# Performance work log

Hardware: AMD Instinct MI355X
Metric: run time of the kernel (lower is better)

The kernel has to match this reference:

```python
import jax, jax.numpy as jnp
import numpy as np

B, L, D, H = 8, 256, 512, 512
NEG_BIG = 1e8  # matches the 100000000.0 mask constant in the original


def setup_inputs() -> dict:
    key = jax.random.key(0)
    k1, k2, k3, k4 = jax.random.split(key, 4)
    enc = jax.random.normal(k1, (B, L, D), dtype=jnp.float32)
    # Glorot-uniform init, matching tf.keras.initializers.GlorotUniform
    s_w = float(np.sqrt(6.0 / (D + H)))
    W_l = jax.random.uniform(k2, (D, H), jnp.float32, -s_w, s_w)
    W_r = jax.random.uniform(k3, (D, H), jnp.float32, -s_w, s_w)
    s_u = float(np.sqrt(6.0 / (H + H)))  # 1-D glorot: fan_in = fan_out = H
    U = jax.random.uniform(k4, (H,), jnp.float32, -s_u, s_u)
    logit_bias = jnp.zeros((1,), jnp.float32)  # bias_initial_value=None -> zeros init
    return {"encoder_output": enc, "W_l": W_l, "W_r": W_r, "U": U, "logit_bias": logit_bias}


def reference(encoder_output, W_l, W_r, U, logit_bias):
    # dot_l[b,i,h], dot_r[b,j,h]
    dot_l = jnp.einsum('bik,kh->bih', encoder_output, W_l)
    dot_r = jnp.einsum('bjk,kh->bjh', encoder_output, W_r)
    # additive biaffine: tanh(dot_l_i + dot_r_j) . U  -> logits[b,i,j]
    final_sum = jnp.tanh(dot_l[:, :, None, :] + dot_r[:, None, :, :])  # [B,L,L,H]
    logits = jnp.einsum('bijh,h->bij', final_sum, U) + logit_bias[0]   # [B,L,L]
    # per-row self-mask (one_hot(i)) applied over all rows at once
    masked = logits - NEG_BIG * jnp.eye(L, dtype=logits.dtype)[None]   # [B,L,L]
    # original returns python lists over i of [B,L]; stack -> [L,B,L]
    mask_scores = jnp.transpose(masked, (1, 0, 2))
    p = jax.nn.sigmoid(mask_scores)
    samples = jax.random.bernoulli(jax.random.key(42), p).astype(jnp.int32)  # [L,B,L]
    # Bernoulli entropy from logits x: p*softplus(-x) + (1-p)*softplus(x)
    entropy = p * jax.nn.softplus(-mask_scores) + (1.0 - p) * jax.nn.softplus(mask_scores)
    return samples, mask_scores, entropy
```

## Files before the change

kernel.cpp:

```cpp
#include <hip/hip_runtime.h>
#include <stdint.h>

#define Bb 8
#define Ll 256
#define Dd 512
#define Hh 512
#define Nout (Ll * Bb * Ll)

#define Kc 2.8853900817779268

#define RNG_PARTITIONABLE 1

typedef __attribute__((ext_vector_type(8))) short bf16x8;
typedef __attribute__((ext_vector_type(4))) float f32x4;

__device__ __forceinline__ uint32_t rotl32(uint32_t v, int s) {
  return (v << s) | (v >> (32 - s));
}
__device__ __forceinline__ void tf_round(uint32_t& x0, uint32_t& x1, int r) {
  x0 += x1;
  x1 = rotl32(x1, r);
  x1 ^= x0;
}
__device__ __forceinline__ uint2 threefry2x32_k042(uint32_t x0, uint32_t x1) {
  const uint32_t k0 = 0u;
  const uint32_t k1 = 42u;
  const uint32_t k2 = 0x1BD11BDAu ^ k0 ^ k1;
  x0 += k0; x1 += k1;
  tf_round(x0, x1, 13); tf_round(x0, x1, 15); tf_round(x0, x1, 26); tf_round(x0, x1, 6);
  x0 += k1; x1 += k2 + 1u;
  tf_round(x0, x1, 17); tf_round(x0, x1, 29); tf_round(x0, x1, 16); tf_round(x0, x1, 24);
  x0 += k2; x1 += k0 + 2u;
  tf_round(x0, x1, 13); tf_round(x0, x1, 15); tf_round(x0, x1, 26); tf_round(x0, x1, 6);
  x0 += k0; x1 += k1 + 3u;
  tf_round(x0, x1, 17); tf_round(x0, x1, 29); tf_round(x0, x1, 16); tf_round(x0, x1, 24);
  x0 += k1; x1 += k2 + 4u;
  tf_round(x0, x1, 13); tf_round(x0, x1, 15); tf_round(x0, x1, 26); tf_round(x0, x1, 6);
  x0 += k2; x1 += k0 + 5u;
  return make_uint2(x0, x1);
}

__device__ __forceinline__ uint32_t rng_bits(uint32_t n) {
#if RNG_PARTITIONABLE
  uint2 o = threefry2x32_k042(0u, n);
  return o.x ^ o.y;
#else
  const uint32_t half = (uint32_t)(Nout / 2);
  if (n < half) {
    uint2 o = threefry2x32_k042(n, n + half);
    return o.x;
  } else {
    uint2 o = threefry2x32_k042(n - half, n);
    return o.y;
  }
#endif
}

__device__ __forceinline__ unsigned short bf16_rne(float f) {
  uint32_t u = __float_as_uint(f);
  u = (u + 0x7fffu + ((u >> 16) & 1u)) >> 16;
  return (unsigned short)u;
}
__device__ __forceinline__ float bf16_tof(unsigned short h) {
  return __uint_as_float(((uint32_t)h) << 16);
}
__device__ __forceinline__ void split3(float a, unsigned short& h,
                                       unsigned short& m, unsigned short& l) {
  h = bf16_rne(a);
  const float r1 = a - bf16_tof(h);
  m = bf16_rne(r1);
  const float r2 = r1 - bf16_tof(m);
  l = bf16_rne(r2);
}

__global__ __launch_bounds__(256) void split_enc(
    const float* __restrict__ enc, unsigned short* __restrict__ ah,
    unsigned short* __restrict__ am, unsigned short* __restrict__ al) {
  const int idx = (blockIdx.x * 256 + threadIdx.x) * 4;
  const float4 v = *(const float4*)(enc + idx);
  ushort4 h4, m4, l4;
  split3(v.x, h4.x, m4.x, l4.x);
  split3(v.y, h4.y, m4.y, l4.y);
  split3(v.z, h4.z, m4.z, l4.z);
  split3(v.w, h4.w, m4.w, l4.w);
  *(ushort4*)(ah + idx) = h4;
  *(ushort4*)(am + idx) = m4;
  *(ushort4*)(al + idx) = l4;
}

__global__ __launch_bounds__(256) void split_wt(
    const float* __restrict__ Wl, const float* __restrict__ Wr,
    unsigned short* __restrict__ wh, unsigned short* __restrict__ wm,
    unsigned short* __restrict__ wl) {
  const int z = blockIdx.z;
  const float* W = z ? Wr : Wl;
  const size_t zo = (size_t)z * Hh * Dd;
  const int k0 = blockIdx.x * 64;
  const int n0 = blockIdx.y * 64;
  __shared__ float tile[64][65];

  const int t = threadIdx.x;
#pragma unroll
  for (int rep = 0; rep < 4; ++rep) {
    const int idx = t + rep * 256;
    const int r = idx >> 4;
    const int c = (idx & 15) * 4;
    const float4 v = *(const float4*)(W + (size_t)(k0 + r) * Hh + n0 + c);
    tile[r][c + 0] = v.x; tile[r][c + 1] = v.y;
    tile[r][c + 2] = v.z; tile[r][c + 3] = v.w;
  }
  __syncthreads();
#pragma unroll
  for (int rep = 0; rep < 4; ++rep) {
    const int idx = t + rep * 256;
    const int rr = idx >> 4;
    const int cc = (idx & 15) * 4;
    ushort4 h4, m4, l4;
    split3(tile[cc + 0][rr], h4.x, m4.x, l4.x);
    split3(tile[cc + 1][rr], h4.y, m4.y, l4.y);
    split3(tile[cc + 2][rr], h4.z, m4.z, l4.z);
    split3(tile[cc + 3][rr], h4.w, m4.w, l4.w);
    const size_t o = zo + (size_t)(n0 + rr) * Dd + k0 + cc;
    *(ushort4*)(wh + o) = h4;
    *(ushort4*)(wm + o) = m4;
    *(ushort4*)(wl + o) = l4;
  }
}

__global__ __launch_bounds__(256) void gemm_mfma(
    const unsigned short* __restrict__ ah, const unsigned short* __restrict__ am,
    const unsigned short* __restrict__ al, const unsigned short* __restrict__ wh,
    const unsigned short* __restrict__ wm, const unsigned short* __restrict__ wl,
    float* __restrict__ el, float* __restrict__ er) {
  const int flat = blockIdx.x;
  const int xcd = flat & 7;
  const int loc = flat >> 3;
  const int z = loc >> 5;
  const int ni = (loc >> 2) & 7;
  const int mi = (xcd << 2) | (loc & 3);
  const size_t zo = (size_t)z * Hh * Dd;
  float* C = z ? er : el;
  const int m0 = mi * 64;
  const int n0 = ni * 64;

  __shared__ unsigned short Asm[3][12 * 512];
  __shared__ unsigned short Bsm[3][12 * 512];

  const int t = threadIdx.x;
  const int lane = t & 63;
  const int wv = t >> 6;
  const int l15 = lane & 15;
  const int kq8 = (lane >> 4) * 8;

  const unsigned short* gp[6];
  size_t go[6];
  int lq[6];
  bool isA[6];
#pragma unroll
  for (int s = 0; s < 6; ++s) {
    const int q = wv * 6 + s;
    if (q < 12) {
      const int p = q >> 2, mt = q & 3;
      gp[s] = (p == 0) ? ah : (p == 1) ? am : al;
      go[s] = (size_t)(m0 + mt * 16 + l15) * Dd + kq8;
      lq[s] = q * 512;
      isA[s] = true;
    } else {
      const int q2 = q - 12;
      const int p = q2 >> 2, nt = q2 & 3;
      gp[s] = (p == 0) ? wh : (p == 1) ? wm : wl;
      go[s] = zo + (size_t)(n0 + nt * 16 + l15) * Dd + kq8;
      lq[s] = q2 * 512;
      isA[s] = false;
    }
  }

  auto stage = [&](int buf, int kc) {
    const int k0 = kc * 32;
#pragma unroll
    for (int s = 0; s < 6; ++s) {
      unsigned short* dst = isA[s] ? &Asm[buf][lq[s]] : &Bsm[buf][lq[s]];
      __builtin_amdgcn_global_load_lds(
          (const __attribute__((address_space(1))) void*)(gp[s] + go[s] + k0),
          (__attribute__((address_space(3))) void*)dst, 16, 0, 0);
    }
  };

  const int mp = wv & 1;
  const int np = wv >> 1;

  f32x4 acc[2][2][2];
#pragma unroll
  for (int mi2 = 0; mi2 < 2; ++mi2)
#pragma unroll
    for (int ni2 = 0; ni2 < 2; ++ni2)
#pragma unroll
      for (int hf = 0; hf < 2; ++hf) acc[mi2][ni2][hf] = (f32x4){0.f, 0.f, 0.f, 0.f};

  stage(0, 0);
  stage(1, 1);

#pragma unroll
  for (int kc = 0; kc < 16; ++kc) {
    const int buf = kc % 3;
    if (kc + 2 < 16) stage((kc + 2) % 3, kc + 2);

    if (kc <= 13) {
      asm volatile("s_waitcnt vmcnt(12)" ::: "memory");
    } else if (kc == 14) {
      asm volatile("s_waitcnt vmcnt(6)" ::: "memory");
    } else {
      asm volatile("s_waitcnt vmcnt(0)" ::: "memory");
    }
    __builtin_amdgcn_s_barrier();
    __builtin_amdgcn_sched_barrier(0);

    bf16x8 af[2][3], bfr[2][3];
#pragma unroll
    for (int mi2 = 0; mi2 < 2; ++mi2)
#pragma unroll
      for (int p = 0; p < 3; ++p)
        af[mi2][p] = *(const bf16x8*)&Asm[buf][(p * 4 + mp * 2 + mi2) * 512 + lane * 8];
#pragma unroll
    for (int ni2 = 0; ni2 < 2; ++ni2)
#pragma unroll
      for (int p = 0; p < 3; ++p)
        bfr[ni2][p] = *(const bf16x8*)&Bsm[buf][(p * 4 + np * 2 + ni2) * 512 + lane * 8];

    const int hf = kc >> 3;
#pragma unroll
    for (int mi2 = 0; mi2 < 2; ++mi2)
#pragma unroll
      for (int ni2 = 0; ni2 < 2; ++ni2) {
        f32x4 A = acc[mi2][ni2][hf];
        A = __builtin_amdgcn_mfma_f32_16x16x32_bf16(af[mi2][0], bfr[ni2][0], A, 0, 0, 0);
        A = __builtin_amdgcn_mfma_f32_16x16x32_bf16(af[mi2][0], bfr[ni2][1], A, 0, 0, 0);
        A = __builtin_amdgcn_mfma_f32_16x16x32_bf16(af[mi2][1], bfr[ni2][0], A, 0, 0, 0);
        A = __builtin_amdgcn_mfma_f32_16x16x32_bf16(af[mi2][0], bfr[ni2][2], A, 0, 0, 0);
        A = __builtin_amdgcn_mfma_f32_16x16x32_bf16(af[mi2][2], bfr[ni2][0], A, 0, 0, 0);
        A = __builtin_amdgcn_mfma_f32_16x16x32_bf16(af[mi2][1], bfr[ni2][1], A, 0, 0, 0);
        acc[mi2][ni2][hf] = A;
      }

    asm volatile("s_waitcnt lgkmcnt(0)" ::: "memory");
    __builtin_amdgcn_sched_barrier(0);
    __builtin_amdgcn_s_barrier();
  }

  const int rbase = (lane >> 4) * 4;
#pragma unroll
  for (int mi2 = 0; mi2 < 2; ++mi2) {
    const int mbase = m0 + (mp * 2 + mi2) * 16 + rbase;
#pragma unroll
    for (int ni2 = 0; ni2 < 2; ++ni2) {
      const int n = n0 + (np * 2 + ni2) * 16 + l15;
#pragma unroll
      for (int reg = 0; reg < 4; ++reg) {
        const double s = (double)acc[mi2][ni2][0][reg] + (double)acc[mi2][ni2][1][reg];
        C[(size_t)(mbase + reg) * Hh + n] = __builtin_amdgcn_exp2f((float)(Kc * s));
      }
    }
  }
}

__device__ __forceinline__ void group4_acc(float& S, const float4 a,
                                           const float4 bv, const float4 u) {
  const float d0 = __builtin_fmaf(a.x, bv.x, 1.0f);
  const float d1 = __builtin_fmaf(a.y, bv.y, 1.0f);
  const float d2 = __builtin_fmaf(a.z, bv.z, 1.0f);
  const float d3 = __builtin_fmaf(a.w, bv.w, 1.0f);
  const float p01 = d0 * d1;
  const float p23 = d2 * d3;
  const float D = p01 * p23;
  float n01 = u.x * d1;
  n01 = __builtin_fmaf(u.y, d0, n01);
  float n23 = u.z * d3;
  n23 = __builtin_fmaf(u.w, d2, n23);
  float num = n01 * p23;
  num = __builtin_fmaf(n23, p01, num);
  S = __builtin_fmaf(num, __builtin_amdgcn_rcpf(D), S);
}

__global__ __launch_bounds__(256) void biaffine_part(
    const float* __restrict__ el, const float* __restrict__ er,
    const float* __restrict__ U, float* __restrict__ part) {
  const int flat = blockIdx.x;
  const int b = flat & 7;
  const int loc = flat >> 3;
  const int ks = loc >> 4;
  const int ib = (loc >> 2) & 3;
  const int jb = loc & 3;
  const int i0 = ib * 64;
  const int j0 = jb * 64;
  const int h0 = ks * 64;

  __shared__ float els[64][68];
  __shared__ float ers[64][68];
  __shared__ float us[64];

  const int t = threadIdx.x;
  if (t < 16) *(float4*)&us[t * 4] = *(const float4*)(U + h0 + t * 4);

  const float* elg = el + (size_t)(b * Ll + i0) * Hh + h0;
  const float* erg = er + (size_t)(b * Ll + j0) * Hh + h0;
#pragma unroll
  for (int rep = 0; rep < 4; ++rep) {
    const int idx = t + rep * 256;
    const int r = idx >> 4;
    const int c = (idx & 15) * 4;
    *(float4*)&els[r][c] = *(const float4*)(elg + (size_t)r * Hh + c);
    *(float4*)&ers[r][c] = *(const float4*)(erg + (size_t)r * Hh + c);
  }
  __syncthreads();

  float usl = 0.0f;
#pragma unroll
  for (int q = 0; q < 16; ++q) {
    const float4 u = *(const float4*)&us[q * 4];
    usl += ((u.x + u.y) + u.z) + u.w;
  }

  const int ti = t >> 4;
  const int tj = t & 15;

  float S[4][4];
#pragma unroll
  for (int r = 0; r < 4; ++r)
#pragma unroll
    for (int c = 0; c < 4; ++c) S[r][c] = 0.0f;

  for (int g = 0; g < 16; ++g) {
    const int h = g * 4;
    const float4 u = *(const float4*)&us[h];
    float4 av[4], bv[4];
#pragma unroll
    for (int c = 0; c < 4; ++c) {
      av[c] = *(const float4*)&els[ti + 16 * c][h];
      bv[c] = *(const float4*)&ers[tj + 16 * c][h];
    }
#pragma unroll
    for (int r = 0; r < 4; ++r)
#pragma unroll
      for (int c = 0; c < 4; ++c) group4_acc(S[r][c], av[r], bv[c], u);
  }

  float* pslice = part + (size_t)ks * Nout;
#pragma unroll
  for (int r = 0; r < 4; ++r) {
    const int i = i0 + ti + 16 * r;
#pragma unroll
    for (int c = 0; c < 4; ++c) {
      const int j = j0 + tj + 16 * c;
      const uint32_t n = ((uint32_t)i * Bb + (uint32_t)b) * Ll + (uint32_t)j;
      pslice[n] = __builtin_fmaf(-2.0f, S[r][c], usl);
    }
  }
}

__global__ __launch_bounds__(256) void biaffine_emit(
    const float* __restrict__ part, const float* __restrict__ biasp,
    float* __restrict__ out) {
  const uint32_t n4 = (blockIdx.x * 256u + threadIdx.x) * 4u;
  double s0 = 0.0, s1 = 0.0, s2 = 0.0, s3 = 0.0;
#pragma unroll
  for (int k = 0; k < 8; ++k) {
    const float4 v = *(const float4*)(part + (size_t)k * Nout + n4);
    s0 += (double)v.x;
    s1 += (double)v.y;
    s2 += (double)v.z;
    s3 += (double)v.w;
  }
  const float bias = biasp[0];
  const double sv[4] = {s0, s1, s2, s3};

  float4 samp4, x4, ent4;
  float* sp = &samp4.x;
  float* xp = &x4.x;
  float* ep = &ent4.x;
#pragma unroll
  for (int q = 0; q < 4; ++q) {
    const uint32_t n = n4 + q;
    const int i = (int)(n >> 11);
    const int j = (int)(n & 255u);
    float x = (float)sv[q] + bias;
    if (i == j) x -= 1e8f;

    const double pd = 1.0 / (1.0 + exp(-(double)x));
    const float pf = (float)pd;

    const uint32_t bits = rng_bits(n);
    const float uu = __uint_as_float((bits >> 9) | 0x3f800000u) - 1.0f;
    sp[q] = (uu < pf) ? 1.0f : 0.0f;
    xp[q] = x;

    const float ax = fabsf(x);
    const float l1p = log1pf(expf(-ax));
    const float sp_pos = fmaxf(x, 0.0f) + l1p;
    const float sp_neg = fmaxf(-x, 0.0f) + l1p;
    ep[q] = pf * sp_neg + (1.0f - pf) * sp_pos;
  }
  *(float4*)(out + n4) = samp4;
  *(float4*)(out + Nout + n4) = x4;
  *(float4*)(out + 2 * (size_t)Nout + n4) = ent4;
}

extern "C" void kernel_launch(void* const* d_in, const int* in_sizes, int n_in,
                              void* d_out, int out_size, void* d_ws,
                              size_t ws_size, hipStream_t stream) {
  const float* enc = (const float*)d_in[0];
  const float* Wl = (const float*)d_in[1];
  const float* Wr = (const float*)d_in[2];
  const float* U = (const float*)d_in[3];
  const float* lb = (const float*)d_in[4];
  float* out = (float*)d_out;

  char* w = (char*)d_ws;
  float* el = (float*)w;                      w += (size_t)Bb * Ll * Hh * 4;
  float* er = (float*)w;                      w += (size_t)Bb * Ll * Hh * 4;
  float* part = (float*)w;                    w += (size_t)8 * Nout * 4;
  unsigned short* ah = (unsigned short*)w;    w += (size_t)Bb * Ll * Dd * 2;
  unsigned short* am = (unsigned short*)w;    w += (size_t)Bb * Ll * Dd * 2;
  unsigned short* al = (unsigned short*)w;    w += (size_t)Bb * Ll * Dd * 2;
  unsigned short* wh = (unsigned short*)w;    w += (size_t)2 * Dd * Hh * 2;
  unsigned short* wm = (unsigned short*)w;    w += (size_t)2 * Dd * Hh * 2;
  unsigned short* wl = (unsigned short*)w;    w += (size_t)2 * Dd * Hh * 2;

  split_enc<<<dim3((Bb * Ll * Dd) / 1024), 256, 0, stream>>>(enc, ah, am, al);
  split_wt<<<dim3(Dd / 64, Hh / 64, 2), 256, 0, stream>>>(Wl, Wr, wh, wm, wl);
  gemm_mfma<<<dim3(512, 1, 1), 256, 0, stream>>>(
      ah, am, al, wh, wm, wl, el, er);
  biaffine_part<<<dim3(1024, 1, 1), 256, 0, stream>>>(el, er, U, part);
  biaffine_emit<<<dim3(Nout / 1024), 256, 0, stream>>>(part, lb, out);
}
```

Before: 125.6 us.

## Split GEMM K dimension across two blocks and combine partials in biaffine kernel

```diff
diff --git a/kernel.cpp b/kernel.cpp
--- a/kernel.cpp
+++ b/kernel.cpp
@@ -6,6 +6,7 @@
 #define Dd 512
 #define Hh 512
 #define Nout (Ll * Bb * Ll)
+#define HALFSZ ((size_t)Bb * Ll * Hh)
 
 #define Kc 2.8853900817779268
 
@@ -131,20 +132,22 @@
     const unsigned short* __restrict__ ah, const unsigned short* __restrict__ am,
     const unsigned short* __restrict__ al, const unsigned short* __restrict__ wh,
     const unsigned short* __restrict__ wm, const unsigned short* __restrict__ wl,
-    float* __restrict__ el, float* __restrict__ er) {
+    float* __restrict__ elp, float* __restrict__ erp) {
   const int flat = blockIdx.x;
   const int xcd = flat & 7;
-  const int loc = flat >> 3;
+  const int half = (flat >> 3) & 1;
+  const int loc = flat >> 4;
   const int z = loc >> 5;
   const int ni = (loc >> 2) & 7;
   const int mi = (xcd << 2) | (loc & 3);
   const size_t zo = (size_t)z * Hh * Dd;
-  float* C = z ? er : el;
+  float* C = (z ? erp : elp) + (size_t)half * HALFSZ;
   const int m0 = mi * 64;
   const int n0 = ni * 64;
-
-  __shared__ unsigned short Asm[3][12 * 512];
-  __shared__ unsigned short Bsm[3][12 * 512];
+  const int kh0 = half * 256;
+
+  __shared__ unsigned short Asm[2][12 * 512];
+  __shared__ unsigned short Bsm[2][12 * 512];
 
   const int t = threadIdx.x;
   const int lane = t & 63;
@@ -176,7 +179,7 @@
   }
 
   auto stage = [&](int buf, int kc) {
-    const int k0 = kc * 32;
+    const int k0 = kh0 + kc * 32;
 #pragma unroll
     for (int s = 0; s < 6; ++s) {
       unsigned short* dst = isA[s] ? &Asm[buf][lq[s]] : &Bsm[buf][lq[s]];
@@ -189,25 +192,20 @@
   const int mp = wv & 1;
   const int np = wv >> 1;
 
-  f32x4 acc[2][2][2];
+  f32x4 acc[2][2];
 #pragma unroll
   for (int mi2 = 0; mi2 < 2; ++mi2)
 #pragma unroll
-    for (int ni2 = 0; ni2 < 2; ++ni2)
-#pragma unroll
-      for (int hf = 0; hf < 2; ++hf) acc[mi2][ni2][hf] = (f32x4){0.f, 0.f, 0.f, 0.f};
+    for (int ni2 = 0; ni2 < 2; ++ni2) acc[mi2][ni2] = (f32x4){0.f, 0.f, 0.f, 0.f};
 
   stage(0, 0);
-  stage(1, 1);
-
-#pragma unroll
-  for (int kc = 0; kc < 16; ++kc) {
-    const int buf = kc % 3;
-    if (kc + 2 < 16) stage((kc + 2) % 3, kc + 2);
-
-    if (kc <= 13) {
-      asm volatile("s_waitcnt vmcnt(12)" ::: "memory");
-    } else if (kc == 14) {
+
+#pragma unroll
+  for (int kc = 0; kc < 8; ++kc) {
+    const int buf = kc & 1;
+    if (kc < 7) stage(buf ^ 1, kc + 1);
+
+    if (kc < 7) {
       asm volatile("s_waitcnt vmcnt(6)" ::: "memory");
     } else {
       asm volatile("s_waitcnt vmcnt(0)" ::: "memory");
@@ -227,19 +225,18 @@
       for (int p = 0; p < 3; ++p)
         bfr[ni2][p] = *(const bf16x8*)&Bsm[buf][(p * 4 + np * 2 + ni2) * 512 + lane * 8];
 
-    const int hf = kc >> 3;
 #pragma unroll
     for (int mi2 = 0; mi2 < 2; ++mi2)
 #pragma unroll
       for (int ni2 = 0; ni2 < 2; ++ni2) {
-        f32x4 A = acc[mi2][ni2][hf];
+        f32x4 A = acc[mi2][ni2];
         A = __builtin_amdgcn_mfma_f32_16x16x32_bf16(af[mi2][0], bfr[ni2][0], A, 0, 0, 0);
         A = __builtin_amdgcn_mfma_f32_16x16x32_bf16(af[mi2][0], bfr[ni2][1], A, 0, 0, 0);
         A = __builtin_amdgcn_mfma_f32_16x16x32_bf16(af[mi2][1], bfr[ni2][0], A, 0, 0, 0);
         A = __builtin_amdgcn_mfma_f32_16x16x32_bf16(af[mi2][0], bfr[ni2][2], A, 0, 0, 0);
         A = __builtin_amdgcn_mfma_f32_16x16x32_bf16(af[mi2][2], bfr[ni2][0], A, 0, 0, 0);
         A = __builtin_amdgcn_mfma_f32_16x16x32_bf16(af[mi2][1], bfr[ni2][1], A, 0, 0, 0);
-        acc[mi2][ni2][hf] = A;
+        acc[mi2][ni2] = A;
       }
 
     asm volatile("s_waitcnt lgkmcnt(0)" ::: "memory");
@@ -255,10 +252,8 @@
     for (int ni2 = 0; ni2 < 2; ++ni2) {
       const int n = n0 + (np * 2 + ni2) * 16 + l15;
 #pragma unroll
-      for (int reg = 0; reg < 4; ++reg) {
-        const double s = (double)acc[mi2][ni2][0][reg] + (double)acc[mi2][ni2][1][reg];
-        C[(size_t)(mbase + reg) * Hh + n] = __builtin_amdgcn_exp2f((float)(Kc * s));
-      }
+      for (int reg = 0; reg < 4; ++reg)
+        C[(size_t)(mbase + reg) * Hh + n] = acc[mi2][ni2][reg];
     }
   }
 }
@@ -281,8 +276,13 @@
   S = __builtin_fmaf(num, __builtin_amdgcn_rcpf(D), S);
 }
 
+__device__ __forceinline__ float combine2(float a0, float a1) {
+  const double s = (double)a0 + (double)a1;
+  return __builtin_amdgcn_exp2f((float)(Kc * s));
+}
+
 __global__ __launch_bounds__(256) void biaffine_part(
-    const float* __restrict__ el, const float* __restrict__ er,
+    const float* __restrict__ elp, const float* __restrict__ erp,
     const float* __restrict__ U, float* __restrict__ part) {
   const int flat = blockIdx.x;
   const int b = flat & 7;
@@ -301,15 +301,25 @@
   const int t = threadIdx.x;
   if (t < 16) *(float4*)&us[t * 4] = *(const float4*)(U + h0 + t * 4);
 
-  const float* elg = el + (size_t)(b * Ll + i0) * Hh + h0;
-  const float* erg = er + (size_t)(b * Ll + j0) * Hh + h0;
+  const float* el0 = elp + (size_t)(b * Ll + i0) * Hh + h0;
+  const float* er0 = erp + (size_t)(b * Ll + j0) * Hh + h0;
 #pragma unroll
   for (int rep = 0; rep < 4; ++rep) {
     const int idx = t + rep * 256;
     const int r = idx >> 4;
     const int c = (idx & 15) * 4;
-    *(float4*)&els[r][c] = *(const float4*)(elg + (size_t)r * Hh + c);
-    *(float4*)&ers[r][c] = *(const float4*)(erg + (size_t)r * Hh + c);
+    const float4 a0 = *(const float4*)(el0 + (size_t)r * Hh + c);
+    const float4 a1 = *(const float4*)(el0 + HALFSZ + (size_t)r * Hh + c);
+    els[r][c + 0] = combine2(a0.x, a1.x);
+    els[r][c + 1] = combine2(a0.y, a1.y);
+    els[r][c + 2] = combine2(a0.z, a1.z);
+    els[r][c + 3] = combine2(a0.w, a1.w);
+    const float4 b0 = *(const float4*)(er0 + (size_t)r * Hh + c);
+    const float4 b1 = *(const float4*)(er0 + HALFSZ + (size_t)r * Hh + c);
+    ers[r][c + 0] = combine2(b0.x, b1.x);
+    ers[r][c + 1] = combine2(b0.y, b1.y);
+    ers[r][c + 2] = combine2(b0.z, b1.z);
+    ers[r][c + 3] = combine2(b0.w, b1.w);
   }
   __syncthreads();
 
@@ -415,8 +425,8 @@
   float* out = (float*)d_out;
 
   char* w = (char*)d_ws;
-  float* el = (float*)w;                      w += (size_t)Bb * Ll * Hh * 4;
-  float* er = (float*)w;                      w += (size_t)Bb * Ll * Hh * 4;
+  float* elp = (float*)w;                     w += 2 * HALFSZ * 4;
+  float* erp = (float*)w;                     w += 2 * HALFSZ * 4;
   float* part = (float*)w;                    w += (size_t)8 * Nout * 4;
   unsigned short* ah = (unsigned short*)w;    w += (size_t)Bb * Ll * Dd * 2;
   unsigned short* am = (unsigned short*)w;    w += (size_t)Bb * Ll * Dd * 2;
@@ -427,8 +437,8 @@
 
   split_enc<<<dim3((Bb * Ll * Dd) / 1024), 256, 0, stream>>>(enc, ah, am, al);
   split_wt<<<dim3(Dd / 64, Hh / 64, 2), 256, 0, stream>>>(Wl, Wr, wh, wm, wl);
-  gemm_mfma<<<dim3(512, 1, 1), 256, 0, stream>>>(
-      ah, am, al, wh, wm, wl, el, er);
-  biaffine_part<<<dim3(1024, 1, 1), 256, 0, stream>>>(el, er, U, part);
+  gemm_mfma<<<dim3(1024, 1, 1), 256, 0, stream>>>(
+      ah, am, al, wh, wm, wl, elp, erp);
+  biaffine_part<<<dim3(1024, 1, 1), 256, 0, stream>>>(elp, erp, U, part);
   biaffine_emit<<<dim3(Nout / 1024), 256, 0, stream>>>(part, lb, out);
 }
```

Result: slower. 128.2 us (+2.1%).
